# Performance work log

Hardware: AMD Instinct MI355X
Metric: run time of the kernel (lower is better)

Reference implementation:

```python
import jax, jax.numpy as jnp
import numpy as np

SIZE = 640
FPN_STRIDES = (8, 16, 32, 64, 128)
REG_MAX = 16
NUM_CLASSES = 80
TOPK = 45


def _build_anchors():
    pts, boxes, strides = [], [], []
    for s in FPN_STRIDES:
        h, w = SIZE // s, SIZE // s
        y, x = np.meshgrid(np.arange(h), np.arange(w), indexing='ij')
        yf = y.ravel().astype(np.float32)
        xf = x.ravel().astype(np.float32)
        pts.append(np.stack([(yf + 0.5) * s, (xf + 0.5) * s], -1))
        boxes.append(np.stack([yf * s, xf * s, (yf + 1) * s, (xf + 1) * s], -1))
        strides.append(np.full(h * w, s, np.float32))
    return (jnp.asarray(np.concatenate(pts), jnp.float32),
            jnp.asarray(np.concatenate(boxes), jnp.float32),
            jnp.asarray(np.concatenate(strides), jnp.float32))


ANCHOR_PTS, ANCHOR_BOXES, STRIDES = _build_anchors()
NUM_ANCHORS = ANCHOR_PTS.shape[0]  # 8525


def _iou(b1, b2):
    # elementwise IoU over trailing dim 4 in (y1, x1, y2, x2); axes are symmetric
    ty = jnp.maximum(b1[..., 0], b2[..., 0])
    tx = jnp.maximum(b1[..., 1], b2[..., 1])
    by = jnp.minimum(b1[..., 2], b2[..., 2])
    bx = jnp.minimum(b1[..., 3], b2[..., 3])
    inter = jnp.clip(by - ty, 0.0) * jnp.clip(bx - tx, 0.0)
    a1 = (b1[..., 2] - b1[..., 0]) * (b1[..., 3] - b1[..., 1])
    a2 = (b2[..., 2] - b2[..., 0]) * (b2[..., 3] - b2[..., 1])
    return inter / (a1 + a2 - inter)


def _assign_single(gt_cls, gt_bbox, pred_d):
    # gt_cls: (N,), gt_bbox: (N,4), pred_d: (4,A)
    A, N, C = NUM_ANCHORS, gt_bbox.shape[0], NUM_CLASSES
    pts, boxes, strides = ANCHOR_PTS, ANCHOR_BOXES, STRIDES
    centers = (gt_bbox[:, :2] + gt_bbox[:, 2:]) / 2
    dist = jnp.linalg.norm(centers[:, None, :] - pts[None, :, :], axis=-1)  # (N,A)
    _, k_ind = jax.lax.top_k(-dist, TOPK)  # (N,K) nearest anchors
    kb = boxes[k_ind]  # (N,K,4)
    Dg = _iou(gt_bbox[:, None, :], kb)  # (N,K)
    tg = Dg.mean(1) + Dg.std(1, ddof=1)  # torch .std() is unbiased
    ap = pts[k_ind]  # (N,K,2)
    inside = ((gt_bbox[:, None, 0] <= ap[..., 0]) & (ap[..., 0] <= gt_bbox[:, None, 2]) &
              (gt_bbox[:, None, 1] <= ap[..., 1]) & (ap[..., 1] <= gt_bbox[:, None, 3]))
    valid = (Dg >= tg[:, None]) & inside  # (N,K)
    n_idx = jnp.broadcast_to(jnp.arange(N, dtype=jnp.int32)[:, None], (N, TOPK))
    pri = jnp.where(valid, n_idx, -1).ravel()
    a_flat = k_ind.ravel()
    win_d = jnp.full((A,), -1, jnp.int32).at[a_flat].max(pri)
    wb = gt_bbox[jnp.clip(win_d, 0)]  # (A,4)
    gt_d = jnp.stack([(pts[:, 0] - wb[:, 0]) / strides,
                      (pts[:, 1] - wb[:, 1]) / strides,
                      (wb[:, 2] - pts[:, 0]) / strides,
                      (wb[:, 3] - pts[:, 1]) / strides], 0)  # (4,A) = [dtop,dleft,dbottom,dright]
    gt_dfl = jnp.where(win_d[None, :] >= 0, gt_d, jnp.inf)
    cls_pair = gt_cls.astype(jnp.int32)[n_idx]  # (N,K)
    ca = (cls_pair * A + k_ind).ravel()
    win_q = jnp.full((C * A,), -1, jnp.int32).at[ca].max(pri).reshape(C, A)
    gbq = gt_bbox[jnp.clip(win_q, 0)]  # (C,A,4)
    # _overlap_tlbr: decode(gt_d)*stride around anchor point, clamped -> clipped gt box
    box1 = jnp.clip(gbq, 0.0, float(SIZE))  # (C,A,4)
    rd = pred_d * strides[None, :]  # (4,A) raw offsets
    box2 = jnp.stack([jnp.clip(pts[:, 0] - rd[0], 0.0, float(SIZE)),
                      jnp.clip(pts[:, 1] - rd[1], 0.0, float(SIZE)),
                      jnp.clip(pts[:, 0] + rd[2], 0.0, float(SIZE)),
                      jnp.clip(pts[:, 1] + rd[3], 0.0, float(SIZE))], -1)  # (A,4)
    q = _iou(box1, box2[None, :, :])  # (C,A)
    gt_qfl = jnp.where(win_q >= 0, q, 0.0)
    return gt_qfl, gt_dfl


def setup_inputs() -> dict:
    key = jax.random.key(0)
    k1, k2, k3, k4 = jax.random.split(key, 4)
    B, N = 16, 64
    tl = jax.random.uniform(k1, (B, N, 2), jnp.float32, 0.0, SIZE - 64.0)
    wh = jax.random.uniform(k2, (B, N, 2), jnp.float32, 16.0, 256.0)
    br = jnp.minimum(tl + wh, float(SIZE))
    gt_bboxes = jnp.concatenate([tl, br], -1)  # (y1,x1,y2,x2)
    gt_clses = jax.random.randint(k3, (B, N), 0, NUM_CLASSES)
    pred_reg = jax.random.normal(k4, (B, 4, REG_MAX + 1, NUM_ANCHORS), jnp.float32)
    return {"gt_clses_batch": gt_clses, "gt_bboxes_batch": gt_bboxes,
            "pred_reg_batch": pred_reg}


def reference(gt_clses_batch, gt_bboxes_batch, pred_reg_batch):
    p = jax.nn.softmax(pred_reg_batch, axis=2)
    rng = jnp.arange(REG_MAX + 1, dtype=p.dtype).reshape(1, 1, -1, 1)
    pred_d = (p * rng).sum(2)  # (B,4,A) integral distribution -> expected offsets
    qfl, dfl = jax.vmap(_assign_single)(gt_clses_batch, gt_bboxes_batch, pred_d)
    return qfl, dfl, ANCHOR_PTS, STRIDES
```

## Files before the change

kernel.cpp:

```cpp
#include <hip/hip_runtime.h>
#include <math.h>
#include <float.h>

#define A_TOTAL 8525
#define NUM_B   16
#define NUM_N   64
#define NUM_C   80
#define K_TOP   45
#define SIZE_F  640.0f

#define UNASSIGNED_SENTINEL 1.0e30f

#define CUTOFF_KEY 0x43000000u
#define NBINS_PAD  2304
#define CAND_MAX   768

#define QFL_FLOATS  ((size_t)NUM_B * NUM_C * A_TOTAL)
#define DFL_FLOATS  ((size_t)NUM_B * 4 * A_TOTAL)
#define MASK_WORDS  (NUM_B * A_TOTAL)
#define MASK_VEC4   ((MASK_WORDS * 2) / 4)
#define QFL_VEC4    (QFL_FLOATS / 4)
#define DFL_VEC4    (DFL_FLOATS / 4)

#define ASSIGN_BLOCKS (NUM_B * NUM_N)

__device__ __forceinline__ void anchor_decode(int a, float& py, float& px, float& s,
                                              float& qy0, float& qx0, float& qy1, float& qx1) {
    int rel, w; float sf;
    if (a < 6400)      { rel = a;        w = 80; sf = 8.f;   }
    else if (a < 8000) { rel = a - 6400; w = 40; sf = 16.f;  }
    else if (a < 8400) { rel = a - 8000; w = 20; sf = 32.f;  }
    else if (a < 8500) { rel = a - 8400; w = 10; sf = 64.f;  }
    else               { rel = a - 8500; w = 5;  sf = 128.f; }
    int y = rel / w, x = rel - y * w;
    float yf = (float)y, xf = (float)x;
    py  = (yf + 0.5f) * sf;  px  = (xf + 0.5f) * sf;
    qy0 = yf * sf;           qx0 = xf * sf;
    qy1 = (yf + 1.f) * sf;   qx1 = (xf + 1.f) * sf;
    s = sf;
}

__device__ __forceinline__ unsigned int dist_key_yx(int yy, int xx, float s,
                                                    float cy, float cx) {
    float py = __fmul_rn(__fadd_rn((float)yy, 0.5f), s);
    float px = __fmul_rn(__fadd_rn((float)xx, 0.5f), s);
    float dy = __fadd_rn(cy, -py);
    float dx = __fadd_rn(cx, -px);
    float v = sqrtf(__fadd_rn(__fmul_rn(dy, dy), __fmul_rn(dx, dx)));
    return __float_as_uint(v);
}

__device__ __forceinline__ float iou_box(float ay0, float ax0, float ay1, float ax1,
                                         float by0, float bx0, float by1, float bx1) {
    float ty = fmaxf(ay0, by0), tx = fmaxf(ax0, bx0);
    float by = fminf(ay1, by1), bx = fminf(ax1, bx1);
    float ih = fmaxf(__fadd_rn(by, -ty), 0.f);
    float iw = fmaxf(__fadd_rn(bx, -tx), 0.f);
    float inter = __fmul_rn(ih, iw);
    float a1 = __fmul_rn(__fadd_rn(ay1, -ay0), __fadd_rn(ax1, -ax0));
    float a2 = __fmul_rn(__fadd_rn(by1, -by0), __fadd_rn(bx1, -bx0));
    return inter / __fadd_rn(__fadd_rn(a1, a2), -inter);
}

__global__ __launch_bounds__(256) void prep_kernel(unsigned long long* __restrict__ mask) {
    size_t gid = (size_t)blockIdx.x * 256 + threadIdx.x;
    size_t nthreads = (size_t)gridDim.x * 256;
    uint4* m4 = (uint4*)mask;
    const uint4 z4 = make_uint4(0u, 0u, 0u, 0u);
    for (size_t i = gid; i < MASK_VEC4; i += nthreads)
        m4[i] = z4;
}

__global__ __launch_bounds__(256) void assign_kernel(const float* __restrict__ gt_bbox,
                                                     unsigned long long* __restrict__ mask,
                                                     float* __restrict__ qfl,
                                                     float* __restrict__ dfl,
                                                     float* __restrict__ opts,
                                                     float* __restrict__ ostr) {
    __shared__ unsigned int hist[NBINS_PAD];
    __shared__ unsigned int wtot[4];
    __shared__ unsigned int cand_key[CAND_MAX];
    __shared__ int          cand_idx[CAND_MAX];
    __shared__ int          s_candn;
    __shared__ int          s_B;
    __shared__ int          sel[K_TOP];
    __shared__ float        dg[K_TOP];
    __shared__ float        s_tg;

    const int   LH[5] = {80, 40, 20, 10, 5};
    const int   LB[5] = {0, 6400, 8000, 8400, 8500};
    const float LS[5] = {8.f, 16.f, 32.f, 64.f, 128.f};

    int tid = threadIdx.x;

    {
        size_t gid = (size_t)blockIdx.x * 256 + tid;
        const size_t nthreads = (size_t)ASSIGN_BLOCKS * 256;

        const uint4 z4 = make_uint4(0u, 0u, 0u, 0u);
        uint4* q4 = (uint4*)qfl;
        for (size_t i = gid; i < QFL_VEC4; i += nthreads)
            q4[i] = z4;

        const unsigned int su = __float_as_uint(UNASSIGNED_SENTINEL);
        const uint4 s4 = make_uint4(su, su, su, su);
        uint4* d4 = (uint4*)dfl;
        for (size_t i = gid; i < DFL_VEC4; i += nthreads)
            d4[i] = s4;

        for (size_t a = gid; a < A_TOTAL; a += nthreads) {
            float py, px, s, q0, q1, q2, q3;
            anchor_decode((int)a, py, px, s, q0, q1, q2, q3);
            opts[2 * a]     = py;
            opts[2 * a + 1] = px;
            ostr[a]         = s;
        }
    }

    int lane = tid & 63, wid = tid >> 6;
    int b = blockIdx.x >> 6;
    int n = blockIdx.x & 63;
    const float* gb = gt_bbox + (size_t)(b * NUM_N + n) * 4;
    float g0 = gb[0], g1 = gb[1], g2 = gb[2], g3 = gb[3];
    float cy = __fmul_rn(__fadd_rn(g0, g2), 0.5f);
    float cx = __fmul_rn(__fadd_rn(g1, g3), 0.5f);

    int wy0[5], wx0[5], wnc[5], wcl[5];
#pragma unroll
    for (int l = 0; l < 5; ++l) {
        float s = LS[l]; int H = LH[l];
        int y0 = (int)((cy - 68.f) / s) - 1; if (y0 < 0) y0 = 0;
        int y1 = (int)((cy + 68.f) / s) + 1; if (y1 > H - 1) y1 = H - 1;
        int x0 = (int)((cx - 68.f) / s) - 1; if (x0 < 0) x0 = 0;
        int x1 = (int)((cx + 68.f) / s) + 1; if (x1 > H - 1) x1 = H - 1;
        wy0[l] = y0; wx0[l] = x0;
        wnc[l] = x1 - x0 + 1;
        wcl[l] = (y1 - y0 + 1) * wnc[l];
    }

    for (int i = tid; i < NBINS_PAD; i += 256) hist[i] = 0u;
    if (tid == 0) s_candn = 0;
    __syncthreads();

#pragma unroll
    for (int l = 0; l < 5; ++l) {
        int nc = wnc[l], cells = wcl[l];
        for (int t = tid; t < cells; t += 256) {
            int r = t / nc, c = t - r * nc;
            unsigned int key = dist_key_yx(wy0[l] + r, wx0[l] + c, LS[l], cy, cx);
            if (key < CUTOFF_KEY) atomicAdd(&hist[key >> 19], 1u);
        }
    }
    __syncthreads();

    unsigned int psum = 0;
    int base = tid * 9;
#pragma unroll
    for (int k = 0; k < 9; ++k) psum += hist[base + k];
    unsigned int x = psum;
    for (int off = 1; off < 64; off <<= 1) {
        unsigned int y = __shfl_up(x, off, 64);
        if (lane >= off) x += y;
    }
    if (lane == 63) wtot[wid] = x;
    __syncthreads();
    unsigned int wbase = 0;
    for (int w = 0; w < 4; ++w) wbase += (w < wid) ? wtot[w] : 0u;
    unsigned int inc = wbase + x;
    unsigned int exc = inc - psum;
    if (exc < (unsigned)K_TOP && inc >= (unsigned)K_TOP) {
        unsigned int cum = exc;
        int bbin = base;
        while (cum + hist[bbin] < (unsigned)K_TOP) { cum += hist[bbin]; ++bbin; }
        s_B = bbin;
    }
    __syncthreads();

    int B = s_B;
#pragma unroll
    for (int l = 0; l < 5; ++l) {
        int nc = wnc[l], cells = wcl[l];
        for (int t = tid; t < cells; t += 256) {
            int r = t / nc, c = t - r * nc;
            int yy = wy0[l] + r, xx = wx0[l] + c;
            unsigned int key = dist_key_yx(yy, xx, LS[l], cy, cx);
            if (key < CUTOFF_KEY && (int)(key >> 19) <= B) {
                int pos = atomicAdd(&s_candn, 1);
                if (pos < CAND_MAX) {
                    cand_key[pos] = key;
                    cand_idx[pos] = LB[l] + yy * LH[l] + xx;
                }
            }
        }
    }
    __syncthreads();

    int M = s_candn < CAND_MAX ? s_candn : CAND_MAX;
    for (int i = tid; i < M; i += 256) {
        unsigned int ki = cand_key[i]; int ii = cand_idx[i];
        int rank = 0;
        for (int j = 0; j < M; ++j) {
            unsigned int kj = cand_key[j]; int ij = cand_idx[j];
            rank += (kj < ki || (kj == ki && ij < ii)) ? 1 : 0;
        }
        if (rank < K_TOP) sel[rank] = ii;
    }
    __syncthreads();

    if (tid < K_TOP) {
        int a = sel[tid];
        float py, px, s, q0, q1, q2, q3;
        anchor_decode(a, py, px, s, q0, q1, q2, q3);
        dg[tid] = iou_box(g0, g1, g2, g3, q0, q1, q2, q3);
    }
    __syncthreads();
    if (tid == 0) {
        float sum = 0.f;
        for (int k = 0; k < K_TOP; ++k) sum = __fadd_rn(sum, dg[k]);
        float mean = sum / (float)K_TOP;
        float ss = 0.f;
        for (int k = 0; k < K_TOP; ++k) {
            float d = __fadd_rn(dg[k], -mean);
            ss = __fadd_rn(ss, __fmul_rn(d, d));
        }
        s_tg = __fadd_rn(mean, sqrtf(ss / (float)(K_TOP - 1)));
    }
    __syncthreads();
    if (tid < K_TOP) {
        int a = sel[tid];
        float py, px, s, q0, q1, q2, q3;
        anchor_decode(a, py, px, s, q0, q1, q2, q3);
        bool inside = (g0 <= py) && (py <= g2) && (g1 <= px) && (px <= g3);
        if (inside && dg[tid] >= s_tg) {
            atomicOr(&mask[(size_t)b * A_TOTAL + a], 1ull << n);
        }
    }
}

__global__ __launch_bounds__(256) void output_kernel(const int* __restrict__ gt_cls,
                                                     const float* __restrict__ gt_bbox,
                                                     const float* __restrict__ pred_reg,
                                                     const unsigned long long* __restrict__ mask,
                                                     float* __restrict__ qfl,
                                                     float* __restrict__ dfl) {
    __shared__ float s_gb[NUM_N * 4];
    __shared__ float s_gc[NUM_N * 4];
    __shared__ int   s_cls[NUM_N];
    __shared__ float s_rd[4][64];

    int tid  = threadIdx.x;
    int lane = tid & 63;
    int d    = tid >> 6;
    int b    = blockIdx.y;
    int a    = blockIdx.x * 64 + lane;

    if (tid < NUM_N * 4) {
        float v = gt_bbox[(size_t)b * NUM_N * 4 + tid];
        s_gb[tid] = v;
        s_gc[tid] = fminf(fmaxf(v, 0.f), SIZE_F);
    }
    if (tid < NUM_N) s_cls[tid] = gt_cls[b * NUM_N + tid];
    __syncthreads();

    unsigned long long m64 = 0ull;
    if (a < A_TOTAL) m64 = mask[(size_t)b * A_TOTAL + a];
    bool active = (m64 != 0ull);

    float py, px, s, q0, q1, q2, q3;
    anchor_decode(a < A_TOTAL ? a : 0, py, px, s, q0, q1, q2, q3);

    if (active) {
        const float* pr = pred_reg + ((size_t)b * 4 + d) * 17 * A_TOTAL + a;
        float xv[17];
#pragma unroll
        for (int j = 0; j < 17; ++j) xv[j] = pr[(size_t)j * A_TOTAL];
        float m = xv[0];
#pragma unroll
        for (int j = 1; j < 17; ++j) m = fmaxf(m, xv[j]);
        float S = 0.f, dot = 0.f;
#pragma unroll
        for (int j = 0; j < 17; ++j) {
            float t = __expf(xv[j] - m);
            S += t;
            dot += t * (float)j;
        }
        s_rd[d][lane] = (dot / S) * s;

        int n = 63 - __clzll(m64);
        const float* g = s_gb + n * 4;
        float v;
        if      (d == 0) v = (py - g[0]) / s;
        else if (d == 1) v = (px - g[1]) / s;
        else if (d == 2) v = (g[2] - py) / s;
        else             v = (g[3] - px) / s;
        dfl[((size_t)b * 4 + d) * A_TOTAL + a] = v;
    }
    __syncthreads();

    if (active && d == 0) {
        float r0 = s_rd[0][lane], r1 = s_rd[1][lane];
        float r2 = s_rd[2][lane], r3 = s_rd[3][lane];
        float b2y0 = fminf(fmaxf(py - r0, 0.f), SIZE_F);
        float b2x0 = fminf(fmaxf(px - r1, 0.f), SIZE_F);
        float b2y1 = fminf(fmaxf(py + r2, 0.f), SIZE_F);
        float b2x1 = fminf(fmaxf(px + r3, 0.f), SIZE_F);

        float* qflp = qfl + (size_t)b * NUM_C * A_TOTAL + a;

        unsigned long long seen0 = 0ull, seen1 = 0ull;
        unsigned long long mm = m64;
        while (mm) {
            int n = 63 - __clzll(mm);
            mm &= ~(1ull << n);
            int c = s_cls[n];
            bool done;
            if (c < 64) {
                unsigned long long bit = 1ull << c;
                done = (seen0 & bit) != 0ull; seen0 |= bit;
            } else {
                unsigned long long bit = 1ull << (c - 64);
                done = (seen1 & bit) != 0ull; seen1 |= bit;
            }
            if (!done) {
                const float* g = s_gc + n * 4;
                qflp[(size_t)c * A_TOTAL] = iou_box(g[0], g[1], g[2], g[3],
                                                    b2y0, b2x0, b2y1, b2x1);
            }
        }
    }
}

extern "C" void kernel_launch(void* const* d_in, const int* in_sizes, int n_in,
                              void* d_out, int out_size, void* d_ws, size_t ws_size,
                              hipStream_t stream) {
    const int*   gt_cls   = (const int*)d_in[0];
    const float* gt_bbox  = (const float*)d_in[1];
    const float* pred_reg = (const float*)d_in[2];

    float* qfl  = (float*)d_out;
    float* dfl  = qfl + QFL_FLOATS;
    float* opts = dfl + DFL_FLOATS;
    float* ostr = opts + (size_t)A_TOTAL * 2;

    unsigned long long* mask = (unsigned long long*)d_ws;

    hipLaunchKernelGGL(prep_kernel, dim3(64), dim3(256), 0, stream, mask);
    hipLaunchKernelGGL(assign_kernel, dim3(ASSIGN_BLOCKS), dim3(256), 0, stream,
                       gt_bbox, mask, qfl, dfl, opts, ostr);
    hipLaunchKernelGGL(output_kernel, dim3((A_TOTAL + 63) / 64, NUM_B), dim3(256), 0, stream,
                       gt_cls, gt_bbox, pred_reg, mask, qfl, dfl);
}
```

Measured before the change: 109.7 us.

## Fuse prep, assign and output kernels into one cooperative kernel with grid syncs

Replaces the three separate launches (mask clear, per-GT assignment, per-anchor output) with a single cooperative mega-kernel that separates the phases with grid-wide barriers. The output phase is handled by a grid-stride loop over anchor tiles. The aim is to remove launch overhead and the gaps between kernels. In exchange it adds two grid syncs, and it relies on all 1024 blocks being co-resident (launch_bounds 256,4); if the cooperative launch fails, it falls back to the old three-kernel path.

Result: slower. 253.3 us (+130.9%).

```diff
diff --git a/kernel.cpp b/kernel.cpp
--- a/kernel.cpp
+++ b/kernel.cpp
@@ -1,6 +1,9 @@
 #include <hip/hip_runtime.h>
+#include <hip/hip_cooperative_groups.h>
 #include <math.h>
 #include <float.h>
+
+namespace cg = cooperative_groups;
 
 #define A_TOTAL 8525
 #define NUM_B   16
@@ -22,7 +25,9 @@
 #define QFL_VEC4    (QFL_FLOATS / 4)
 #define DFL_VEC4    (DFL_FLOATS / 4)
 
-#define ASSIGN_BLOCKS (NUM_B * NUM_N)
+#define GRID_BLOCKS   (NUM_B * NUM_N)
+#define NUM_AGROUPS   ((A_TOTAL + 63) / 64)
+#define TILES         (NUM_AGROUPS * NUM_B)
 
 __device__ __forceinline__ void anchor_decode(int a, float& py, float& px, float& s,
                                               float& qy0, float& qx0, float& qy1, float& qx1) {
@@ -62,13 +67,279 @@
     return inter / __fadd_rn(__fadd_rn(a1, a2), -inter);
 }
 
+__global__ __launch_bounds__(256, 4) void mega_kernel(const int* __restrict__ gt_cls,
+                                                      const float* __restrict__ gt_bbox,
+                                                      const float* __restrict__ pred_reg,
+                                                      unsigned long long* __restrict__ mask,
+                                                      float* __restrict__ qfl,
+                                                      float* __restrict__ dfl,
+                                                      float* __restrict__ opts,
+                                                      float* __restrict__ ostr) {
+    __shared__ unsigned int hist[NBINS_PAD];
+    __shared__ unsigned int wtot[4];
+    __shared__ unsigned int cand_key[CAND_MAX];
+    __shared__ int          cand_idx[CAND_MAX];
+    __shared__ int          s_candn;
+    __shared__ int          s_B;
+    __shared__ int          sel[K_TOP];
+    __shared__ float        dg[K_TOP];
+    __shared__ float        s_tg;
+    __shared__ float        s_gb[NUM_N * 4];
+    __shared__ float        s_gc[NUM_N * 4];
+    __shared__ int          s_cls[NUM_N];
+    __shared__ float        s_rd[4][64];
+
+    cg::grid_group gridg = cg::this_grid();
+
+    const int tid = threadIdx.x;
+    const int bid = blockIdx.x;
+    const size_t nthreads = (size_t)GRID_BLOCKS * 256;
+    const size_t gid = (size_t)bid * 256 + tid;
+
+    {
+        uint4* m4 = (uint4*)mask;
+        const uint4 z4 = make_uint4(0u, 0u, 0u, 0u);
+        for (size_t i = gid; i < MASK_VEC4; i += nthreads) m4[i] = z4;
+    }
+    gridg.sync();
+
+    {
+        const uint4 z4 = make_uint4(0u, 0u, 0u, 0u);
+        uint4* q4 = (uint4*)qfl;
+        for (size_t i = gid; i < QFL_VEC4; i += nthreads) q4[i] = z4;
+
+        const unsigned int su = __float_as_uint(UNASSIGNED_SENTINEL);
+        const uint4 s4 = make_uint4(su, su, su, su);
+        uint4* d4 = (uint4*)dfl;
+        for (size_t i = gid; i < DFL_VEC4; i += nthreads) d4[i] = s4;
+
+        for (size_t a = gid; a < A_TOTAL; a += nthreads) {
+            float py, px, s, q0, q1, q2, q3;
+            anchor_decode((int)a, py, px, s, q0, q1, q2, q3);
+            opts[2 * a]     = py;
+            opts[2 * a + 1] = px;
+            ostr[a]         = s;
+        }
+    }
+
+    {
+        const int   LH[5] = {80, 40, 20, 10, 5};
+        const int   LB[5] = {0, 6400, 8000, 8400, 8500};
+        const float LS[5] = {8.f, 16.f, 32.f, 64.f, 128.f};
+
+        int lane = tid & 63, wid = tid >> 6;
+        int b = bid >> 6;
+        int n = bid & 63;
+        const float* gb = gt_bbox + (size_t)(b * NUM_N + n) * 4;
+        float g0 = gb[0], g1 = gb[1], g2 = gb[2], g3 = gb[3];
+        float cy = __fmul_rn(__fadd_rn(g0, g2), 0.5f);
+        float cx = __fmul_rn(__fadd_rn(g1, g3), 0.5f);
+
+        int wy0[5], wx0[5], wnc[5], wcl[5];
+#pragma unroll
+        for (int l = 0; l < 5; ++l) {
+            float s = LS[l]; int H = LH[l];
+            int y0 = (int)((cy - 68.f) / s) - 1; if (y0 < 0) y0 = 0;
+            int y1 = (int)((cy + 68.f) / s) + 1; if (y1 > H - 1) y1 = H - 1;
+            int x0 = (int)((cx - 68.f) / s) - 1; if (x0 < 0) x0 = 0;
+            int x1 = (int)((cx + 68.f) / s) + 1; if (x1 > H - 1) x1 = H - 1;
+            wy0[l] = y0; wx0[l] = x0;
+            wnc[l] = x1 - x0 + 1;
+            wcl[l] = (y1 - y0 + 1) * wnc[l];
+        }
+
+        for (int i = tid; i < NBINS_PAD; i += 256) hist[i] = 0u;
+        if (tid == 0) s_candn = 0;
+        __syncthreads();
+
+#pragma unroll
+        for (int l = 0; l < 5; ++l) {
+            int nc = wnc[l], cells = wcl[l];
+            for (int t = tid; t < cells; t += 256) {
+                int r = t / nc, c = t - r * nc;
+                unsigned int key = dist_key_yx(wy0[l] + r, wx0[l] + c, LS[l], cy, cx);
+                if (key < CUTOFF_KEY) atomicAdd(&hist[key >> 19], 1u);
+            }
+        }
+        __syncthreads();
+
+        unsigned int psum = 0;
+        int base = tid * 9;
+#pragma unroll
+        for (int k = 0; k < 9; ++k) psum += hist[base + k];
+        unsigned int x = psum;
+        for (int off = 1; off < 64; off <<= 1) {
+            unsigned int y = __shfl_up(x, off, 64);
+            if (lane >= off) x += y;
+        }
+        if (lane == 63) wtot[wid] = x;
+        __syncthreads();
+        unsigned int wbase = 0;
+        for (int w = 0; w < 4; ++w) wbase += (w < wid) ? wtot[w] : 0u;
+        unsigned int inc = wbase + x;
+        unsigned int exc = inc - psum;
+        if (exc < (unsigned)K_TOP && inc >= (unsigned)K_TOP) {
+            unsigned int cum = exc;
+            int bbin = base;
+            while (cum + hist[bbin] < (unsigned)K_TOP) { cum += hist[bbin]; ++bbin; }
+            s_B = bbin;
+        }
+        __syncthreads();
+
+        int B = s_B;
+#pragma unroll
+        for (int l = 0; l < 5; ++l) {
+            int nc = wnc[l], cells = wcl[l];
+            for (int t = tid; t < cells; t += 256) {
+                int r = t / nc, c = t - r * nc;
+                int yy = wy0[l] + r, xx = wx0[l] + c;
+                unsigned int key = dist_key_yx(yy, xx, LS[l], cy, cx);
+                if (key < CUTOFF_KEY && (int)(key >> 19) <= B) {
+                    int pos = atomicAdd(&s_candn, 1);
+                    if (pos < CAND_MAX) {
+                        cand_key[pos] = key;
+                        cand_idx[pos] = LB[l] + yy * LH[l] + xx;
+                    }
+                }
+            }
+        }
+        __syncthreads();
+
+        int M = s_candn < CAND_MAX ? s_candn : CAND_MAX;
+        for (int i = tid; i < M; i += 256) {
+            unsigned int ki = cand_key[i]; int ii = cand_idx[i];
+            int rank = 0;
+            for (int j = 0; j < M; ++j) {
+                unsigned int kj = cand_key[j]; int ij = cand_idx[j];
+                rank += (kj < ki || (kj == ki && ij < ii)) ? 1 : 0;
+            }
+            if (rank < K_TOP) sel[rank] = ii;
+        }
+        __syncthreads();
+
+        if (tid < K_TOP) {
+            int a = sel[tid];
+            float py, px, s, q0, q1, q2, q3;
+            anchor_decode(a, py, px, s, q0, q1, q2, q3);
+            dg[tid] = iou_box(g0, g1, g2, g3, q0, q1, q2, q3);
+        }
+        __syncthreads();
+        if (tid == 0) {
+            float sum = 0.f;
+            for (int k = 0; k < K_TOP; ++k) sum = __fadd_rn(sum, dg[k]);
+            float mean = sum / (float)K_TOP;
+            float ss = 0.f;
+            for (int k = 0; k < K_TOP; ++k) {
+                float d = __fadd_rn(dg[k], -mean);
+                ss = __fadd_rn(ss, __fmul_rn(d, d));
+            }
+            s_tg = __fadd_rn(mean, sqrtf(ss / (float)(K_TOP - 1)));
+        }
+        __syncthreads();
+        if (tid < K_TOP) {
+            int a = sel[tid];
+            float py, px, s, q0, q1, q2, q3;
+            anchor_decode(a, py, px, s, q0, q1, q2, q3);
+            bool inside = (g0 <= py) && (py <= g2) && (g1 <= px) && (px <= g3);
+            if (inside && dg[tid] >= s_tg) {
+                atomicOr(&mask[(size_t)b * A_TOTAL + a], 1ull << n);
+            }
+        }
+    }
+
+    gridg.sync();
+
+    for (int t = bid; t < TILES; t += GRID_BLOCKS) {
+        int b = t / NUM_AGROUPS;
+        int g = t - b * NUM_AGROUPS;
+        int lane = tid & 63;
+        int d    = tid >> 6;
+        int a    = g * 64 + lane;
+
+        __syncthreads();
+        if (tid < NUM_N * 4) {
+            float v = gt_bbox[(size_t)b * NUM_N * 4 + tid];
+            s_gb[tid] = v;
+            s_gc[tid] = fminf(fmaxf(v, 0.f), SIZE_F);
+        }
+        if (tid < NUM_N) s_cls[tid] = gt_cls[b * NUM_N + tid];
+        __syncthreads();
+
+        unsigned long long m64 = 0ull;
+        if (a < A_TOTAL) m64 = mask[(size_t)b * A_TOTAL + a];
+        bool active = (m64 != 0ull);
+
+        float py, px, s, q0, q1, q2, q3;
+        anchor_decode(a < A_TOTAL ? a : 0, py, px, s, q0, q1, q2, q3);
+
+        if (active) {
+            const float* pr = pred_reg + ((size_t)b * 4 + d) * 17 * A_TOTAL + a;
+            float xv[17];
+#pragma unroll
+            for (int j = 0; j < 17; ++j) xv[j] = pr[(size_t)j * A_TOTAL];
+            float m = xv[0];
+#pragma unroll
+            for (int j = 1; j < 17; ++j) m = fmaxf(m, xv[j]);
+            float S = 0.f, dot = 0.f;
+#pragma unroll
+            for (int j = 0; j < 17; ++j) {
+                float tt = __expf(xv[j] - m);
+                S += tt;
+                dot += tt * (float)j;
+            }
+            s_rd[d][lane] = (dot / S) * s;
+
+            int n = 63 - __clzll(m64);
+            const float* gg = s_gb + n * 4;
+            float v;
+            if      (d == 0) v = (py - gg[0]) / s;
+            else if (d == 1) v = (px - gg[1]) / s;
+            else if (d == 2) v = (gg[2] - py) / s;
+            else             v = (gg[3] - px) / s;
+            dfl[((size_t)b * 4 + d) * A_TOTAL + a] = v;
+        }
+        __syncthreads();
+
+        if (active && d == 0) {
+            float r0 = s_rd[0][lane], r1 = s_rd[1][lane];
+            float r2 = s_rd[2][lane], r3 = s_rd[3][lane];
+            float b2y0 = fminf(fmaxf(py - r0, 0.f), SIZE_F);
+            float b2x0 = fminf(fmaxf(px - r1, 0.f), SIZE_F);
+            float b2y1 = fminf(fmaxf(py + r2, 0.f), SIZE_F);
+            float b2x1 = fminf(fmaxf(px + r3, 0.f), SIZE_F);
+
+            float* qflp = qfl + (size_t)b * NUM_C * A_TOTAL + a;
+
+            unsigned long long seen0 = 0ull, seen1 = 0ull;
+            unsigned long long mm = m64;
+            while (mm) {
+                int n = 63 - __clzll(mm);
+                mm &= ~(1ull << n);
+                int c = s_cls[n];
+                bool done;
+                if (c < 64) {
+                    unsigned long long bit = 1ull << c;
+                    done = (seen0 & bit) != 0ull; seen0 |= bit;
+                } else {
+                    unsigned long long bit = 1ull << (c - 64);
+                    done = (seen1 & bit) != 0ull; seen1 |= bit;
+                }
+                if (!done) {
+                    const float* gg = s_gc + n * 4;
+                    qflp[(size_t)c * A_TOTAL] = iou_box(gg[0], gg[1], gg[2], gg[3],
+                                                        b2y0, b2x0, b2y1, b2x1);
+                }
+            }
+        }
+    }
+}
+
 __global__ __launch_bounds__(256) void prep_kernel(unsigned long long* __restrict__ mask) {
     size_t gid = (size_t)blockIdx.x * 256 + threadIdx.x;
     size_t nthreads = (size_t)gridDim.x * 256;
     uint4* m4 = (uint4*)mask;
     const uint4 z4 = make_uint4(0u, 0u, 0u, 0u);
-    for (size_t i = gid; i < MASK_VEC4; i += nthreads)
-        m4[i] = z4;
+    for (size_t i = gid; i < MASK_VEC4; i += nthreads) m4[i] = z4;
 }
 
 __global__ __launch_bounds__(256) void assign_kernel(const float* __restrict__ gt_bbox,
@@ -92,28 +363,20 @@
     const float LS[5] = {8.f, 16.f, 32.f, 64.f, 128.f};
 
     int tid = threadIdx.x;
-
     {
         size_t gid = (size_t)blockIdx.x * 256 + tid;
-        const size_t nthreads = (size_t)ASSIGN_BLOCKS * 256;
-
+        const size_t nthreads = (size_t)GRID_BLOCKS * 256;
         const uint4 z4 = make_uint4(0u, 0u, 0u, 0u);
         uint4* q4 = (uint4*)qfl;
-        for (size_t i = gid; i < QFL_VEC4; i += nthreads)
-            q4[i] = z4;
-
+        for (size_t i = gid; i < QFL_VEC4; i += nthreads) q4[i] = z4;
         const unsigned int su = __float_as_uint(UNASSIGNED_SENTINEL);
         const uint4 s4 = make_uint4(su, su, su, su);
         uint4* d4 = (uint4*)dfl;
-        for (size_t i = gid; i < DFL_VEC4; i += nthreads)
-            d4[i] = s4;
-
+        for (size_t i = gid; i < DFL_VEC4; i += nthreads) d4[i] = s4;
         for (size_t a = gid; a < A_TOTAL; a += nthreads) {
             float py, px, s, q0, q1, q2, q3;
             anchor_decode((int)a, py, px, s, q0, q1, q2, q3);
-            opts[2 * a]     = py;
-            opts[2 * a + 1] = px;
-            ostr[a]         = s;
+            opts[2 * a] = py; opts[2 * a + 1] = px; ostr[a] = s;
         }
     }
 
@@ -344,9 +607,16 @@
 
     unsigned long long* mask = (unsigned long long*)d_ws;
 
-    hipLaunchKernelGGL(prep_kernel, dim3(64), dim3(256), 0, stream, mask);
-    hipLaunchKernelGGL(assign_kernel, dim3(ASSIGN_BLOCKS), dim3(256), 0, stream,
-                       gt_bbox, mask, qfl, dfl, opts, ostr);
-    hipLaunchKernelGGL(output_kernel, dim3((A_TOTAL + 63) / 64, NUM_B), dim3(256), 0, stream,
-                       gt_cls, gt_bbox, pred_reg, mask, qfl, dfl);
-}
+    void* args[] = { (void*)&gt_cls, (void*)&gt_bbox, (void*)&pred_reg, (void*)&mask,
+                     (void*)&qfl, (void*)&dfl, (void*)&opts, (void*)&ostr };
+    hipError_t err = hipLaunchCooperativeKernel((const void*)mega_kernel,
+                                                dim3(GRID_BLOCKS), dim3(256),
+                                                args, 0, stream);
+    if (err != hipSuccess) {
+        hipLaunchKernelGGL(prep_kernel, dim3(64), dim3(256), 0, stream, mask);
+        hipLaunchKernelGGL(assign_kernel, dim3(GRID_BLOCKS), dim3(256), 0, stream,
+                           gt_bbox, mask, qfl, dfl, opts, ostr);
+        hipLaunchKernelGGL(output_kernel, dim3(NUM_AGROUPS, NUM_B), dim3(256), 0, stream,
+                           gt_cls, gt_bbox, pred_reg, mask, qfl, dfl);
+    }
+}
```

## Move qfl zeroing and dfl sentinel fill into output kernel tile stores

Applied to the files above, without the earlier changes.

The qfl zero-fill and dfl sentinel fill move out of the assign kernel and into the output kernel. Each output block now clears its own 80x64 qfl tile and writes either the computed dfl value or the sentinel per anchor. Anchor point and stride output moves into the prep kernel. This stops assign blocks from streaming about 44 MB of fills before their real work, and avoids a separate pass over dfl. The output kernel now does more stores per block, and those qfl stores are strided by A_TOTAL per class.

Result: slower. 112.3 us (+2.4%).

```diff
diff --git a/kernel.cpp b/kernel.cpp
--- a/kernel.cpp
+++ b/kernel.cpp
@@ -19,10 +19,8 @@
 #define DFL_FLOATS  ((size_t)NUM_B * 4 * A_TOTAL)
 #define MASK_WORDS  (NUM_B * A_TOTAL)
 #define MASK_VEC4   ((MASK_WORDS * 2) / 4)
-#define QFL_VEC4    (QFL_FLOATS / 4)
-#define DFL_VEC4    (DFL_FLOATS / 4)
-
-#define ASSIGN_BLOCKS (NUM_B * NUM_N)
+
+#define NUM_AGROUPS ((A_TOTAL + 63) / 64)
 
 __device__ __forceinline__ void anchor_decode(int a, float& py, float& px, float& s,
                                               float& qy0, float& qx0, float& qy1, float& qx1) {
@@ -62,21 +60,25 @@
     return inter / __fadd_rn(__fadd_rn(a1, a2), -inter);
 }
 
-__global__ __launch_bounds__(256) void prep_kernel(unsigned long long* __restrict__ mask) {
+__global__ __launch_bounds__(256) void prep_kernel(unsigned long long* __restrict__ mask,
+                                                   float* __restrict__ opts,
+                                                   float* __restrict__ ostr) {
     size_t gid = (size_t)blockIdx.x * 256 + threadIdx.x;
     size_t nthreads = (size_t)gridDim.x * 256;
     uint4* m4 = (uint4*)mask;
     const uint4 z4 = make_uint4(0u, 0u, 0u, 0u);
-    for (size_t i = gid; i < MASK_VEC4; i += nthreads)
-        m4[i] = z4;
+    for (size_t i = gid; i < MASK_VEC4; i += nthreads) m4[i] = z4;
+    for (size_t a = gid; a < A_TOTAL; a += nthreads) {
+        float py, px, s, q0, q1, q2, q3;
+        anchor_decode((int)a, py, px, s, q0, q1, q2, q3);
+        opts[2 * a]     = py;
+        opts[2 * a + 1] = px;
+        ostr[a]         = s;
+    }
 }
 
 __global__ __launch_bounds__(256) void assign_kernel(const float* __restrict__ gt_bbox,
-                                                     unsigned long long* __restrict__ mask,
-                                                     float* __restrict__ qfl,
-                                                     float* __restrict__ dfl,
-                                                     float* __restrict__ opts,
-                                                     float* __restrict__ ostr) {
+                                                     unsigned long long* __restrict__ mask) {
     __shared__ unsigned int hist[NBINS_PAD];
     __shared__ unsigned int wtot[4];
     __shared__ unsigned int cand_key[CAND_MAX];
@@ -92,31 +94,6 @@
     const float LS[5] = {8.f, 16.f, 32.f, 64.f, 128.f};
 
     int tid = threadIdx.x;
-
-    {
-        size_t gid = (size_t)blockIdx.x * 256 + tid;
-        const size_t nthreads = (size_t)ASSIGN_BLOCKS * 256;
-
-        const uint4 z4 = make_uint4(0u, 0u, 0u, 0u);
-        uint4* q4 = (uint4*)qfl;
-        for (size_t i = gid; i < QFL_VEC4; i += nthreads)
-            q4[i] = z4;
-
-        const unsigned int su = __float_as_uint(UNASSIGNED_SENTINEL);
-        const uint4 s4 = make_uint4(su, su, su, su);
-        uint4* d4 = (uint4*)dfl;
-        for (size_t i = gid; i < DFL_VEC4; i += nthreads)
-            d4[i] = s4;
-
-        for (size_t a = gid; a < A_TOTAL; a += nthreads) {
-            float py, px, s, q0, q1, q2, q3;
-            anchor_decode((int)a, py, px, s, q0, q1, q2, q3);
-            opts[2 * a]     = py;
-            opts[2 * a + 1] = px;
-            ostr[a]         = s;
-        }
-    }
-
     int lane = tid & 63, wid = tid >> 6;
     int b = blockIdx.x >> 6;
     int n = blockIdx.x & 63;
@@ -252,7 +229,8 @@
     int lane = tid & 63;
     int d    = tid >> 6;
     int b    = blockIdx.y;
-    int a    = blockIdx.x * 64 + lane;
+    int a0   = blockIdx.x * 64;
+    int a    = a0 + lane;
 
     if (tid < NUM_N * 4) {
         float v = gt_bbox[(size_t)b * NUM_N * 4 + tid];
@@ -260,6 +238,16 @@
         s_gc[tid] = fminf(fmaxf(v, 0.f), SIZE_F);
     }
     if (tid < NUM_N) s_cls[tid] = gt_cls[b * NUM_N + tid];
+
+    {
+        float* qb = qfl + (size_t)b * NUM_C * A_TOTAL + a0;
+#pragma unroll
+        for (int it = 0; it < (NUM_C * 64) / 256; ++it) {
+            int idx = it * 256 + tid;
+            int c = idx >> 6, la = idx & 63;
+            if (a0 + la < A_TOTAL) qb[(size_t)c * A_TOTAL + la] = 0.f;
+        }
+    }
     __syncthreads();
 
     unsigned long long m64 = 0ull;
@@ -269,30 +257,32 @@
     float py, px, s, q0, q1, q2, q3;
     anchor_decode(a < A_TOTAL ? a : 0, py, px, s, q0, q1, q2, q3);
 
-    if (active) {
-        const float* pr = pred_reg + ((size_t)b * 4 + d) * 17 * A_TOTAL + a;
-        float xv[17];
-#pragma unroll
-        for (int j = 0; j < 17; ++j) xv[j] = pr[(size_t)j * A_TOTAL];
-        float m = xv[0];
-#pragma unroll
-        for (int j = 1; j < 17; ++j) m = fmaxf(m, xv[j]);
-        float S = 0.f, dot = 0.f;
-#pragma unroll
-        for (int j = 0; j < 17; ++j) {
-            float t = __expf(xv[j] - m);
-            S += t;
-            dot += t * (float)j;
-        }
-        s_rd[d][lane] = (dot / S) * s;
-
-        int n = 63 - __clzll(m64);
-        const float* g = s_gb + n * 4;
-        float v;
-        if      (d == 0) v = (py - g[0]) / s;
-        else if (d == 1) v = (px - g[1]) / s;
-        else if (d == 2) v = (g[2] - py) / s;
-        else             v = (g[3] - px) / s;
+    if (a < A_TOTAL) {
+        float v = UNASSIGNED_SENTINEL;
+        if (active) {
+            const float* pr = pred_reg + ((size_t)b * 4 + d) * 17 * A_TOTAL + a;
+            float xv[17];
+#pragma unroll
+            for (int j = 0; j < 17; ++j) xv[j] = pr[(size_t)j * A_TOTAL];
+            float m = xv[0];
+#pragma unroll
+            for (int j = 1; j < 17; ++j) m = fmaxf(m, xv[j]);
+            float S = 0.f, dot = 0.f;
+#pragma unroll
+            for (int j = 0; j < 17; ++j) {
+                float t = __expf(xv[j] - m);
+                S += t;
+                dot += t * (float)j;
+            }
+            s_rd[d][lane] = (dot / S) * s;
+
+            int n = 63 - __clzll(m64);
+            const float* g = s_gb + n * 4;
+            if      (d == 0) v = (py - g[0]) / s;
+            else if (d == 1) v = (px - g[1]) / s;
+            else if (d == 2) v = (g[2] - py) / s;
+            else             v = (g[3] - px) / s;
+        }
         dfl[((size_t)b * 4 + d) * A_TOTAL + a] = v;
     }
     __syncthreads();
@@ -344,9 +334,9 @@
 
     unsigned long long* mask = (unsigned long long*)d_ws;
 
-    hipLaunchKernelGGL(prep_kernel, dim3(64), dim3(256), 0, stream, mask);
-    hipLaunchKernelGGL(assign_kernel, dim3(ASSIGN_BLOCKS), dim3(256), 0, stream,
-                       gt_bbox, mask, qfl, dfl, opts, ostr);
-    hipLaunchKernelGGL(output_kernel, dim3((A_TOTAL + 63) / 64, NUM_B), dim3(256), 0, stream,
+    hipLaunchKernelGGL(prep_kernel, dim3(64), dim3(256), 0, stream, mask, opts, ostr);
+    hipLaunchKernelGGL(assign_kernel, dim3(NUM_B * NUM_N), dim3(256), 0, stream,
+                       gt_bbox, mask);
+    hipLaunchKernelGGL(output_kernel, dim3(NUM_AGROUPS, NUM_B), dim3(256), 0, stream,
                        gt_cls, gt_bbox, pred_reg, mask, qfl, dfl);
 }
```
